# Kernel optimization log

Measured on AMD Instinct MI355X. Metric: run time of the kernel, lower is better.

Reference implementation:

```python
import jax, jax.numpy as jnp
import numpy as np

N, E, G = 100000, 500000, 1000


def _gat(h_in, src, dst, W, a_s, a_d, b, n):
    # PyG GATConv, heads=1, concat=True, negative_slope=0.2, self-loops already in src/dst
    h = h_in @ W.T                                  # [N, out]
    alpha_src = h @ a_s                             # [N]
    alpha_dst = h @ a_d                             # [N]
    e = jax.nn.leaky_relu(alpha_src[src] + alpha_dst[dst], 0.2)  # [E']
    m = jax.ops.segment_max(e, dst, num_segments=n)
    ex = jnp.exp(e - m[dst])
    den = jax.ops.segment_sum(ex, dst, num_segments=n)
    alpha = ex / den[dst]                           # segment softmax over incoming edges
    out = jax.ops.segment_sum(h[src] * alpha[:, None], dst, num_segments=n)
    return out + b


def _forward(x, edge_index, batch, w1, b1, w2, b2, w3, b3,
             g1w, g1as, g1ad, g1b, g2w, g2as, g2ad, g2b,
             g3w, g3as, g3ad, g3b, g4w, g4as, g4ad, g4b,
             g5w, g5as, g5ad, g5b, lw, lb):
    n = x.shape[0]
    h = jax.nn.relu(x @ w1.T + b1)
    h = jax.nn.relu(h @ w2.T + b2)
    h = jax.nn.relu(h @ w3.T + b3)
    loops = jnp.arange(n)
    src = jnp.concatenate([edge_index[0], loops])   # add self-loops
    dst = jnp.concatenate([edge_index[1], loops])
    h = jax.nn.relu(_gat(h, src, dst, g1w, g1as, g1ad, g1b, n))
    h = jax.nn.relu(_gat(h, src, dst, g2w, g2as, g2ad, g2b, n))
    h = jax.nn.relu(_gat(h, src, dst, g3w, g3as, g3ad, g3b, n))
    h = jax.nn.relu(_gat(h, src, dst, g4w, g4as, g4ad, g4b, n))
    h = jax.nn.relu(_gat(h, src, dst, g5w, g5as, g5ad, g5b, n))
    sums = jax.ops.segment_sum(h, batch, num_segments=G)            # [G,32]
    cnt = jax.ops.segment_sum(jnp.ones((n,), h.dtype), batch, num_segments=G)
    mean = sums / jnp.maximum(cnt, 1.0)[:, None]
    return jax.nn.sigmoid(mean @ lw.T + lb)         # [G,1]


def setup_inputs() -> dict:
    key = jax.random.key(0)
    ks = jax.random.split(key, 24)

    def lin(k, o, i):
        k1, k2 = jax.random.split(k)
        s = 1.0 / np.sqrt(i)
        return (jax.random.uniform(k1, (o, i), jnp.float32, -s, s),
                jax.random.uniform(k2, (o,), jnp.float32, -s, s))

    def gat_p(k, i, o):
        k1, k2, k3 = jax.random.split(k, 3)
        s = 1.0 / np.sqrt(i)
        W = jax.random.uniform(k1, (o, i), jnp.float32, -s, s)
        a_s = jax.random.normal(k2, (o,), jnp.float32) / np.sqrt(o)
        a_d = jax.random.normal(k3, (o,), jnp.float32) / np.sqrt(o)
        return W, a_s, a_d, jnp.zeros((o,), jnp.float32)

    inp = {}
    inp['x'] = jax.random.normal(ks[0], (N, 1), jnp.float32)
    inp['edge_index'] = jax.random.randint(ks[1], (2, E), 0, N)
    inp['batch'] = jnp.sort(jax.random.randint(ks[2], (N,), 0, G))
    inp['w1'], inp['b1'] = lin(ks[3], 16, 1)
    inp['w2'], inp['b2'] = lin(ks[4], 32, 16)
    inp['w3'], inp['b3'] = lin(ks[5], 64, 32)
    dims = [(64, 128), (128, 256), (256, 128), (128, 64), (64, 32)]
    for j, (i, o) in enumerate(dims, start=1):
        W, a_s, a_d, b = gat_p(ks[5 + j], i, o)
        inp[f'g{j}w'], inp[f'g{j}as'], inp[f'g{j}ad'], inp[f'g{j}b'] = W, a_s, a_d, b
    inp['lw'], inp['lb'] = lin(ks[12], 1, 32)
    return inp


def reference(x, edge_index, batch, w1, b1, w2, b2, w3, b3,
              g1w, g1as, g1ad, g1b, g2w, g2as, g2ad, g2b,
              g3w, g3as, g3ad, g3b, g4w, g4as, g4ad, g4b,
              g5w, g5as, g5ad, g5b, lw, lb):
    return _forward(x, edge_index, batch, w1, b1, w2, b2, w3, b3,
                    g1w, g1as, g1ad, g1b, g2w, g2as, g2ad, g2b,
                    g3w, g3as, g3ad, g3b, g4w, g4as, g4ad, g4b,
                    g5w, g5as, g5ad, g5b, lw, lb)
```

## Files before the change

kernel.cpp:

```cpp
#include <hip/hip_runtime.h>
#include <math.h>

typedef __attribute__((ext_vector_type(8))) __bf16 bf16x8;
typedef __attribute__((ext_vector_type(4))) float f32x4;

__device__ inline unsigned short f2bf(float f) {
    unsigned int i = __float_as_uint(f);
    unsigned int r = i + 0x7fffu + ((i >> 16) & 1u);
    return (unsigned short)(r >> 16);
}
__device__ inline float bf2f(unsigned short u) {
    return __uint_as_float(((unsigned int)u) << 16);
}

__global__ __launch_bounds__(256) void mlp_kernel(
    const float* __restrict__ x,
    const float* __restrict__ w1, const float* __restrict__ b1,
    const float* __restrict__ w2, const float* __restrict__ b2,
    const float* __restrict__ w3, const float* __restrict__ b3,
    unsigned short* __restrict__ h0, int n,
    const float* __restrict__ g0,
    const float* __restrict__ as1, const float* __restrict__ ad1,
    float* __restrict__ s1out, float* __restrict__ d1out) {
    int tid = threadIdx.x;
    __shared__ float4 sw1q[4], sb1q[4];
    __shared__ float4 sw2q[128];
    __shared__ float4 sw3q[512];
    __shared__ float2 psd1[64];
    __shared__ float sb2l[32], sb3l[64];
    __shared__ float pres[4][64], predu[4][64];
    {
        int ii = tid & 63, ch = tid >> 6;
        const float* gp = g0 + (size_t)(ch * 32) * 64 + ii;
        float s = 0.f, d = 0.f;
#pragma unroll 4
        for (int o = 0; o < 32; o++) {
            float w = gp[o * 64];
            s += as1[ch * 32 + o] * w;
            d += ad1[ch * 32 + o] * w;
        }
        pres[ch][ii] = s;
        predu[ch][ii] = d;
    }
    if (tid < 4) { sw1q[tid] = ((const float4*)w1)[tid]; sb1q[tid] = ((const float4*)b1)[tid]; }
    if (tid >= 32 && tid < 64) sb2l[tid - 32] = b2[tid - 32];
    if (tid >= 64 && tid < 128) sb3l[tid - 64] = b3[tid - 64];
    for (int i = tid; i < 128; i += 256) sw2q[i] = ((const float4*)w2)[i];
    for (int i = tid; i < 512; i += 256) sw3q[i] = ((const float4*)w3)[i];
    __syncthreads();
    if (tid < 64) {
        psd1[tid] = make_float2(pres[0][tid] + pres[1][tid] + pres[2][tid] + pres[3][tid],
                                predu[0][tid] + predu[1][tid] + predu[2][tid] + predu[3][tid]);
    }
    __syncthreads();
    int node = blockIdx.x * 256 + tid;
    if (node >= n) return;
    float xv = x[node];
    float t1[16], t2[32];
#pragma unroll
    for (int q = 0; q < 4; q++) {
        float4 wv = sw1q[q], bv = sb1q[q];
        t1[q * 4 + 0] = fmaxf(wv.x * xv + bv.x, 0.f);
        t1[q * 4 + 1] = fmaxf(wv.y * xv + bv.y, 0.f);
        t1[q * 4 + 2] = fmaxf(wv.z * xv + bv.z, 0.f);
        t1[q * 4 + 3] = fmaxf(wv.w * xv + bv.w, 0.f);
    }
#pragma unroll
    for (int o = 0; o < 32; o++) {
        float a = sb2l[o];
#pragma unroll
        for (int q = 0; q < 4; q++) {
            float4 wv = sw2q[o * 4 + q];
            a += wv.x * t1[q * 4] + wv.y * t1[q * 4 + 1] + wv.z * t1[q * 4 + 2] +
                 wv.w * t1[q * 4 + 3];
        }
        t2[o] = fmaxf(a, 0.f);
    }
    float sdot = 0.f, ddot = 0.f;
    uint4* gp = (uint4*)(h0 + (size_t)node * 64);
#pragma unroll
    for (int c = 0; c < 8; c++) {
        unsigned int wvec[4];
#pragma unroll
        for (int p = 0; p < 4; p++) {
            int o = c * 8 + p * 2;
            float a0 = sb3l[o], a1 = sb3l[o + 1];
#pragma unroll
            for (int q = 0; q < 8; q++) {
                float4 wa = sw3q[o * 8 + q];
                float4 wb = sw3q[(o + 1) * 8 + q];
                a0 += wa.x * t2[q * 4] + wa.y * t2[q * 4 + 1] + wa.z * t2[q * 4 + 2] +
                      wa.w * t2[q * 4 + 3];
                a1 += wb.x * t2[q * 4] + wb.y * t2[q * 4 + 1] + wb.z * t2[q * 4 + 2] +
                      wb.w * t2[q * 4 + 3];
            }
            float r0 = fmaxf(a0, 0.f), r1 = fmaxf(a1, 0.f);
            float2 q0 = psd1[o], q1 = psd1[o + 1];
            sdot += r0 * q0.x + r1 * q1.x;
            ddot += r0 * q0.y + r1 * q1.y;
            wvec[p] = (unsigned)f2bf(r0) | ((unsigned)f2bf(r1) << 16);
        }
        gp[c] = make_uint4(wvec[0], wvec[1], wvec[2], wvec[3]);
    }
    s1out[node] = sdot;
    d1out[node] = ddot;
}

__global__ __launch_bounds__(256) void misc_kernel(
    const float* __restrict__ g0, const float* __restrict__ g1, const float* __restrict__ g2,
    const float* __restrict__ g3, const float* __restrict__ g4,
    unsigned short* __restrict__ wbAll,
    const int* __restrict__ batch, int* __restrict__ gstart, int G, int n,
    const int* __restrict__ dst, int* __restrict__ deg, int E,
    int f2bfB, int gsB, int histB,
    const float* __restrict__ as2, const float* __restrict__ ad2,
    float* __restrict__ pv2) {
    int b = blockIdx.x;
    int tid = threadIdx.x;
    if (b < f2bfB) {
        int i = b * 256 + tid;
        float v;
        if (i < 8192) v = g0[i];
        else if (i < 40960) v = g1[i - 8192];
        else if (i < 73728) v = g2[i - 40960];
        else if (i < 81920) v = g3[i - 73728];
        else if (i < 83968) v = g4[i - 81920];
        else return;
        wbAll[i] = f2bf(v);
    } else if (b < f2bfB + gsB) {
        int g = (b - f2bfB) * 256 + tid;
        if (g > G) return;
        if (g == G) { gstart[G] = n; return; }
        int lo = 0, hi = n;
        while (lo < hi) {
            int mid = (lo + hi) >> 1;
            if (batch[mid] < g) lo = mid + 1;
            else hi = mid;
        }
        gstart[g] = lo;
    } else if (b < f2bfB + gsB + histB) {
        int e = (b - f2bfB - gsB) * 256 + tid;
        if (e >= E) return;
        atomicAdd(&deg[dst[e]], 1);
    } else {
        if (tid < 128) {
            float s = 0.f;
            for (int o = 0; o < 256; o++) s += as2[o] * g1[o * 128 + tid];
            pv2[tid] = s;
        } else {
            int c = tid - 128;
            float s = 0.f;
            for (int o = 0; o < 256; o++) s += ad2[o] * g1[o * 128 + c];
            pv2[128 + c] = s;
        }
    }
}

template <int K, int BN, int EPI>
__global__ __launch_bounds__(256) void gemm_mfma(
    const unsigned short* __restrict__ A, const unsigned short* __restrict__ Wb,
    unsigned short* __restrict__ Cb,
    const float* __restrict__ avs, const float* __restrict__ avd,
    float* __restrict__ as_, float* __restrict__ ad_,
    const float* __restrict__ bias, int n, int O) {
    constexpr int SN = BN / 32;
    constexpr int K8 = K / 8;
    __shared__ unsigned short As[128][K + 8];
    __shared__ unsigned short Ws[BN][72];
    int tid = threadIdx.x;
    int row0 = blockIdx.x * 128;
    int w = tid >> 6, lane = tid & 63;
    int wr = w >> 1, wc = w & 1;
    int quad = lane >> 4, l15 = lane & 15;

    for (int i = tid; i < 128 * K8; i += 256) {
        int r = i / K8, c8 = i % K8;
        int gr = row0 + r;
        uint4 v = make_uint4(0u, 0u, 0u, 0u);
        if (gr < n) v = *(const uint4*)(A + (size_t)gr * K + c8 * 8);
        *(uint4*)&As[r][c8 * 8] = v;
    }

    for (int ot = 0; ot * BN < O; ot++) {
        int col0 = ot * BN;
        f32x4 acc[4][SN];
#pragma unroll
        for (int mi = 0; mi < 4; mi++)
#pragma unroll
            for (int ni = 0; ni < SN; ni++) acc[mi][ni] = (f32x4){0.f, 0.f, 0.f, 0.f};
#pragma unroll 1
        for (int k0 = 0; k0 < K; k0 += 64) {
#pragma unroll
            for (int i = tid; i < BN * 8; i += 256) {
                int r = i >> 3, c8 = i & 7;
                uint4 v = *(const uint4*)(Wb + (size_t)(col0 + r) * K + k0 + c8 * 8);
                *(uint4*)&Ws[r][c8 * 8] = v;
            }
            __syncthreads();
#pragma unroll
            for (int kk = 0; kk < 64; kk += 32) {
                bf16x8 bfr[SN];
#pragma unroll
                for (int ni = 0; ni < SN; ni++)
                    bfr[ni] = *(const bf16x8*)&Ws[wc * (BN / 2) + ni * 16 + l15][kk + quad * 8];
#pragma unroll
                for (int mi = 0; mi < 4; mi++) {
                    bf16x8 afr = *(const bf16x8*)&As[wr * 64 + mi * 16 + l15][k0 + kk + quad * 8];
#pragma unroll
                    for (int ni = 0; ni < SN; ni++)
                        acc[mi][ni] = __builtin_amdgcn_mfma_f32_16x16x32_bf16(
                            afr, bfr[ni], acc[mi][ni], 0, 0, 0);
                }
            }
            __syncthreads();
        }
        float avsv[SN], avdv[SN], bv[SN];
        int gc[SN];
#pragma unroll
        for (int ni = 0; ni < SN; ni++) {
            gc[ni] = col0 + wc * (BN / 2) + ni * 16 + l15;
            if constexpr (EPI != 2) {
                avsv[ni] = avs[gc[ni]];
                avdv[ni] = avd[gc[ni]];
            }
            if constexpr (EPI >= 1) bv[ni] = bias[gc[ni]];
        }
#pragma unroll
        for (int mi = 0; mi < 4; mi++) {
            int gm0 = row0 + wr * 64 + mi * 16 + quad * 4;
            float ps[4] = {0.f, 0.f, 0.f, 0.f}, pd[4] = {0.f, 0.f, 0.f, 0.f};
#pragma unroll
            for (int ni = 0; ni < SN; ni++) {
#pragma unroll
                for (int r = 0; r < 4; r++) {
                    float d = acc[mi][ni][r];
                    if constexpr (EPI >= 1) d = fmaxf(d + bv[ni], 0.f);
                    int gm = gm0 + r;
                    if (gm < n) Cb[(size_t)gm * O + gc[ni]] = f2bf(d);
                    if constexpr (EPI != 2) {
                        ps[r] += d * avsv[ni];
                        pd[r] += d * avdv[ni];
                    }
                }
            }
            if constexpr (EPI != 2) {
#pragma unroll
                for (int r = 0; r < 4; r++) {
#pragma unroll
                    for (int m = 1; m <= 8; m <<= 1) {
                        ps[r] += __shfl_xor(ps[r], m);
                        pd[r] += __shfl_xor(pd[r], m);
                    }
                }
                if (l15 == 0) {
#pragma unroll
                    for (int r = 0; r < 4; r++) {
                        int gm = gm0 + r;
                        if (gm < n) {
                            atomicAdd(&as_[gm], ps[r]);
                            atomicAdd(&ad_[gm], pd[r]);
                        }
                    }
                }
            }
        }
    }
}

__global__ void scan_block_sums(const int* __restrict__ deg, int* __restrict__ bsums, int n) {
    __shared__ int sdata[256];
    int tid = threadIdx.x;
    int base = blockIdx.x * 1024 + tid * 4;
    int s = 0;
    for (int i = 0; i < 4; i++) {
        int g = base + i;
        if (g < n) s += deg[g] + 1;
    }
    sdata[tid] = s;
    __syncthreads();
    for (int off = 128; off > 0; off >>= 1) {
        if (tid < off) sdata[tid] += sdata[tid + off];
        __syncthreads();
    }
    if (tid == 0) bsums[blockIdx.x] = sdata[0];
}

__global__ void scan_write(const int* __restrict__ deg, const int* __restrict__ bsums,
                           int* __restrict__ rowptr, int* __restrict__ cursor,
                           int* __restrict__ esrc, int n, int nb) {
    __shared__ int sdata[256];
    int tid = threadIdx.x;
    sdata[tid] = (tid < blockIdx.x && tid < nb) ? bsums[tid] : 0;
    __syncthreads();
    for (int off = 128; off > 0; off >>= 1) {
        if (tid < off) sdata[tid] += sdata[tid + off];
        __syncthreads();
    }
    int base = sdata[0];
    __syncthreads();
    int gbase = blockIdx.x * 1024 + tid * 4;
    int v[4];
    int s = 0;
    for (int i = 0; i < 4; i++) {
        int g = gbase + i;
        v[i] = (g < n) ? deg[g] + 1 : 0;
        s += v[i];
    }
    sdata[tid] = s;
    __syncthreads();
    for (int off = 1; off < 256; off <<= 1) {
        int t = (tid >= off) ? sdata[tid - off] : 0;
        __syncthreads();
        sdata[tid] += t;
        __syncthreads();
    }
    int excl = sdata[tid] - s + base;
    for (int i = 0; i < 4; i++) {
        int g = gbase + i;
        if (g < n) {
            rowptr[g] = excl;
            esrc[excl] = g;
            cursor[g] = excl + 1;
        }
        excl += v[i];
    }
    if (blockIdx.x == gridDim.x - 1 && tid == 255) rowptr[n] = base + sdata[255];
}

__global__ void scatter_kernel(const int* __restrict__ esrc_in, const int* __restrict__ edst_in,
                               int* __restrict__ cursor, int* __restrict__ esrc, int E) {
    int e = blockIdx.x * 256 + threadIdx.x;
    if (e >= E) return;
    int pos = atomicAdd(&cursor[edst_in[e]], 1);
    esrc[pos] = esrc_in[e];
}

template <int O, bool BIASRELU>
__global__ __launch_bounds__(256) void gat_aggregate(
    const unsigned short* __restrict__ hl, const float* __restrict__ as_,
    const float* __restrict__ ad_, const int* __restrict__ rowptr,
    const int* __restrict__ esrc, const float* __restrict__ bias,
    unsigned short* __restrict__ hout, int n, float* __restrict__ zeroBuf, int zeroCnt) {
    int gtid = blockIdx.x * 256 + threadIdx.x;
    if (gtid < zeroCnt) zeroBuf[gtid] = 0.f;
    constexpr int C8 = O / 8;
    constexpr int EPP = 16 / C8;
    int tid = threadIdx.x;
    int v = blockIdx.x * 16 + (tid >> 4);
    int l = tid & 15;
    int gbase = tid & 48;
    if (v >= n) return;
    int beg = rowptr[v], end = rowptr[v + 1];
    int deg = end - beg;
    float adv = ad_[v];
    int sub = l / C8;
    int c = l % C8;
    float acc[8] = {0.f, 0.f, 0.f, 0.f, 0.f, 0.f, 0.f, 0.f};
    if (deg <= 16) {
        int sreg = v;
        float e = -1e30f;
        if (l < deg) {
            sreg = esrc[beg + l];
            float t = as_[sreg] + adv;
            e = (t > 0.f) ? t : 0.2f * t;
        }
        float m = e;
#pragma unroll
        for (int o = 8; o > 0; o >>= 1) m = fmaxf(m, __shfl_xor(m, o));
        float ex = (l < deg) ? __expf(e - m) : 0.f;
        float sum = ex;
#pragma unroll
        for (int o = 8; o > 0; o >>= 1) sum += __shfl_xor(sum, o);
        float alpha_r = ex / sum;
        for (int j0 = 0; j0 < deg; j0 += EPP) {
            int idx = j0 + sub;
            int cidx = (idx < deg) ? idx : 0;
            float alpha = __shfl(alpha_r, gbase + cidx);
            int s2 = __shfl(sreg, gbase + cidx);
            if (idx >= deg) alpha = 0.f;
            uint4 raw = ((const uint4*)(hl + (size_t)s2 * O))[c];
            acc[0] += alpha * __uint_as_float(raw.x << 16);
            acc[1] += alpha * __uint_as_float(raw.x & 0xffff0000u);
            acc[2] += alpha * __uint_as_float(raw.y << 16);
            acc[3] += alpha * __uint_as_float(raw.y & 0xffff0000u);
            acc[4] += alpha * __uint_as_float(raw.z << 16);
            acc[5] += alpha * __uint_as_float(raw.z & 0xffff0000u);
            acc[6] += alpha * __uint_as_float(raw.w << 16);
            acc[7] += alpha * __uint_as_float(raw.w & 0xffff0000u);
        }
    } else {
        float mymax = -1e30f;
        for (int j = beg + l; j < end; j += 16) {
            float e = as_[esrc[j]] + adv;
            e = (e > 0.f) ? e : 0.2f * e;
            mymax = fmaxf(mymax, e);
        }
#pragma unroll
        for (int o = 8; o > 0; o >>= 1) mymax = fmaxf(mymax, __shfl_xor(mymax, o));
        float mysum = 0.f;
        for (int j = beg + l; j < end; j += 16) {
            float e = as_[esrc[j]] + adv;
            e = (e > 0.f) ? e : 0.2f * e;
            mysum += __expf(e - mymax);
        }
#pragma unroll
        for (int o = 8; o > 0; o >>= 1) mysum += __shfl_xor(mysum, o);
        float invden = 1.f / mysum;
        for (int j0 = beg; j0 < end; j0 += EPP) {
            int j = j0 + sub;
            bool valid = j < end;
            int s = valid ? esrc[j] : v;
            float e = as_[s] + adv;
            e = (e > 0.f) ? e : 0.2f * e;
            float alpha = valid ? __expf(e - mymax) * invden : 0.f;
            uint4 raw = ((const uint4*)(hl + (size_t)s * O))[c];
            acc[0] += alpha * __uint_as_float(raw.x << 16);
            acc[1] += alpha * __uint_as_float(raw.x & 0xffff0000u);
            acc[2] += alpha * __uint_as_float(raw.y << 16);
            acc[3] += alpha * __uint_as_float(raw.y & 0xffff0000u);
            acc[4] += alpha * __uint_as_float(raw.z << 16);
            acc[5] += alpha * __uint_as_float(raw.z & 0xffff0000u);
            acc[6] += alpha * __uint_as_float(raw.w << 16);
            acc[7] += alpha * __uint_as_float(raw.w & 0xffff0000u);
        }
    }
#pragma unroll
    for (int o = C8; o < 16; o <<= 1)
#pragma unroll
        for (int k = 0; k < 8; k++) acc[k] += __shfl_xor(acc[k], o);
    if (l < C8) {
        unsigned short ov[8];
#pragma unroll
        for (int k = 0; k < 8; k++) {
            float val = acc[k];
            if constexpr (BIASRELU) val = fmaxf(val + bias[c * 8 + k], 0.f);
            ov[k] = f2bf(val);
        }
        uint4 packed;
        packed.x = (unsigned)ov[0] | ((unsigned)ov[1] << 16);
        packed.y = (unsigned)ov[2] | ((unsigned)ov[3] << 16);
        packed.z = (unsigned)ov[4] | ((unsigned)ov[5] << 16);
        packed.w = (unsigned)ov[6] | ((unsigned)ov[7] << 16);
        ((uint4*)(hout + (size_t)v * O))[c] = packed;
    }
}

__global__ __launch_bounds__(256) void pool_final_kernel(
    const unsigned short* __restrict__ h, const int* __restrict__ start,
    const float* __restrict__ lw, const float* __restrict__ lb,
    float* __restrict__ out, int G) {
    __shared__ float red[8][33];
    int g = blockIdx.x;
    if (g >= G) return;
    int beg = start[g], end = start[g + 1];
    int tid = threadIdx.x;
    int nodeLane = tid >> 5, f = tid & 31;
    float acc = 0.f;
    for (int v = beg + nodeLane; v < end; v += 8)
        acc += bf2f(h[(size_t)v * 32 + f]);
    red[nodeLane][f] = acc;
    __syncthreads();
    if (tid < 32) {
        float s = 0.f;
#pragma unroll
        for (int i = 0; i < 8; i++) s += red[i][f];
        float inv = 1.f / fmaxf((float)(end - beg), 1.f);
        float val = s * inv * lw[f];
#pragma unroll
        for (int o = 16; o > 0; o >>= 1) val += __shfl_xor(val, o);
        if (f == 0) out[g] = 1.f / (1.f + __expf(-(val + lb[0])));
    }
}

extern "C" void kernel_launch(void* const* d_in, const int* in_sizes, int n_in,
                              void* d_out, int out_size, void* d_ws, size_t ws_size,
                              hipStream_t stream) {
    const float* x = (const float*)d_in[0];
    const int* ei = (const int*)d_in[1];
    const int* batch = (const int*)d_in[2];
    const float* w1 = (const float*)d_in[3];
    const float* b1 = (const float*)d_in[4];
    const float* w2 = (const float*)d_in[5];
    const float* b2 = (const float*)d_in[6];
    const float* w3 = (const float*)d_in[7];
    const float* b3 = (const float*)d_in[8];
    const float* gw[5];
    const float* gas[5];
    const float* gad[5];
    const float* gb[5];
    for (int l = 0; l < 5; l++) {
        gw[l] = (const float*)d_in[9 + l * 4 + 0];
        gas[l] = (const float*)d_in[9 + l * 4 + 1];
        gad[l] = (const float*)d_in[9 + l * 4 + 2];
        gb[l] = (const float*)d_in[9 + l * 4 + 3];
    }
    const float* lw = (const float*)d_in[29];
    const float* lb = (const float*)d_in[30];
    float* out = (float*)d_out;

    int N = in_sizes[0];
    int E = in_sizes[1] / 2;
    int G = out_size;
    int Etot = E + N;

    char* ws = (char*)d_ws;
    size_t off = 0;
    auto alloc = [&](size_t bytes) -> void* {
        void* p = ws + off;
        off = (off + bytes + 255) & ~(size_t)255;
        return p;
    };
    unsigned short* actA = (unsigned short*)alloc((size_t)N * 256 * 2);
    unsigned short* actB = (unsigned short*)alloc((size_t)N * 256 * 2);
    char* zblock = (char*)alloc((size_t)N * 20);
    float* sd2 = (float*)zblock;
    float* sd3 = sd2 + (size_t)N * 2;
    int* deg = (int*)(zblock + (size_t)N * 16);
    float* sd1 = (float*)alloc((size_t)N * 2 * 4);
    float* pv2 = (float*)alloc(256 * 4);
    int* rowptr = (int*)alloc((size_t)(N + 1) * 4);
    int* cursor = (int*)alloc((size_t)(N + 1) * 4);
    int* esrc = (int*)alloc((size_t)Etot * 4);
    int* bsums = (int*)alloc(4096);
    int* gstart = (int*)alloc((size_t)(G + 1) * 4);
    unsigned short* wbAll = (unsigned short*)alloc((size_t)83968 * 2);
    const int woff[5] = {0, 8192, 40960, 73728, 81920};
    unsigned short* wb[5];
    for (int l = 0; l < 5; l++) wb[l] = wbAll + woff[l];
    (void)ws_size;
    (void)n_in;

    hipMemsetAsync(zblock, 0, (size_t)N * 20, stream);

    int f2bfB = (83968 + 255) / 256;
    int gsB = (G + 1 + 255) / 256;
    int histB = (E + 255) / 256;
    misc_kernel<<<f2bfB + gsB + histB + 1, 256, 0, stream>>>(
        gw[0], gw[1], gw[2], gw[3], gw[4], wbAll, batch, gstart, G, N, ei + E, deg, E,
        f2bfB, gsB, histB, gas[1], gad[1], pv2);

    mlp_kernel<<<(N + 255) / 256, 256, 0, stream>>>(x, w1, b1, w2, b2, w3, b3, actA, N,
                                                    gw[0], gas[0], gad[0], sd1, sd1 + N);

    int nb = (N + 1023) / 1024;
    scan_block_sums<<<nb, 256, 0, stream>>>(deg, bsums, N);
    scan_write<<<nb, 256, 0, stream>>>(deg, bsums, rowptr, cursor, esrc, N, nb);
    scatter_kernel<<<(E + 255) / 256, 256, 0, stream>>>(ei, ei + E, cursor, esrc, E);

    int aggBlocks = (N + 15) / 16;
    int gx = (N + 127) / 128;

    gat_aggregate<64, false><<<aggBlocks, 256, 0, stream>>>(
        actA, sd1, sd1 + N, rowptr, esrc, nullptr, actB, N, nullptr, 0);
    gemm_mfma<64, 64, 1><<<gx, 256, 0, stream>>>(actB, wb[0], actA, pv2, pv2 + 128, sd2,
                                                 sd2 + N, gb[0], N, 128);

    gat_aggregate<128, false><<<aggBlocks, 256, 0, stream>>>(
        actA, sd2, sd2 + N, rowptr, esrc, nullptr, actB, N, sd1, 2 * N);
    gemm_mfma<128, 64, 2><<<gx, 256, 0, stream>>>(actB, wb[1], actA, nullptr, nullptr,
                                                  nullptr, nullptr, gb[1], N, 256);

    gemm_mfma<256, 64, 0><<<gx, 256, 0, stream>>>(actA, wb[2], actB, gas[2], gad[2], sd3,
                                                  sd3 + N, nullptr, N, 128);
    gat_aggregate<128, true><<<aggBlocks, 256, 0, stream>>>(
        actB, sd3, sd3 + N, rowptr, esrc, gb[2], actA, N, sd2, 2 * N);

    gemm_mfma<128, 64, 0><<<gx, 256, 0, stream>>>(actA, wb[3], actB, gas[3], gad[3], sd1,
                                                  sd1 + N, nullptr, N, 64);
    gat_aggregate<64, true><<<aggBlocks, 256, 0, stream>>>(
        actB, sd1, sd1 + N, rowptr, esrc, gb[3], actA, N, nullptr, 0);

    gemm_mfma<64, 32, 0><<<gx, 256, 0, stream>>>(actA, wb[4], actB, gas[4], gad[4], sd2,
                                                 sd2 + N, nullptr, N, 32);
    gat_aggregate<32, true><<<aggBlocks, 256, 0, stream>>>(
        actB, sd2, sd2 + N, rowptr, esrc, gb[4], actA, N, nullptr, 0);

    pool_final_kernel<<<G, 256, 0, stream>>>(actA, gstart, lw, lb, out, G);
}
```

Before: 500.9 us.

## Split GEMM output columns across grid.y and stream A tiles per K step

The GEMM kernel used to load a whole 128xK A tile into shared memory once and then loop over all output column tiles inside a single block. It now assigns one column tile per block through a 2D grid and streams 64-wide A chunks per K step. The goal is more blocks in flight and a smaller LDS footprint, which should raise occupancy for the wide layers. In exchange, A is re-read from global memory once per column tile, and K is now a runtime argument rather than a template constant.

```diff
diff --git a/kernel.cpp b/kernel.cpp
--- a/kernel.cpp
+++ b/kernel.cpp
@@ -156,110 +156,105 @@
     }
 }
 
-template <int K, int BN, int EPI>
+template <int BN, int EPI>
 __global__ __launch_bounds__(256) void gemm_mfma(
     const unsigned short* __restrict__ A, const unsigned short* __restrict__ Wb,
     unsigned short* __restrict__ Cb,
     const float* __restrict__ avs, const float* __restrict__ avd,
     float* __restrict__ as_, float* __restrict__ ad_,
-    const float* __restrict__ bias, int n, int O) {
+    const float* __restrict__ bias, int n, int K, int O) {
     constexpr int SN = BN / 32;
-    constexpr int K8 = K / 8;
-    __shared__ unsigned short As[128][K + 8];
+    __shared__ unsigned short As[128][72];
     __shared__ unsigned short Ws[BN][72];
     int tid = threadIdx.x;
-    int row0 = blockIdx.x * 128;
+    int row0 = blockIdx.x * 128, col0 = blockIdx.y * BN;
     int w = tid >> 6, lane = tid & 63;
     int wr = w >> 1, wc = w & 1;
     int quad = lane >> 4, l15 = lane & 15;
-
-    for (int i = tid; i < 128 * K8; i += 256) {
-        int r = i / K8, c8 = i % K8;
-        int gr = row0 + r;
-        uint4 v = make_uint4(0u, 0u, 0u, 0u);
-        if (gr < n) v = *(const uint4*)(A + (size_t)gr * K + c8 * 8);
-        *(uint4*)&As[r][c8 * 8] = v;
-    }
-
-    for (int ot = 0; ot * BN < O; ot++) {
-        int col0 = ot * BN;
-        f32x4 acc[4][SN];
-#pragma unroll
-        for (int mi = 0; mi < 4; mi++)
-#pragma unroll
-            for (int ni = 0; ni < SN; ni++) acc[mi][ni] = (f32x4){0.f, 0.f, 0.f, 0.f};
-#pragma unroll 1
-        for (int k0 = 0; k0 < K; k0 += 64) {
-#pragma unroll
-            for (int i = tid; i < BN * 8; i += 256) {
-                int r = i >> 3, c8 = i & 7;
-                uint4 v = *(const uint4*)(Wb + (size_t)(col0 + r) * K + k0 + c8 * 8);
-                *(uint4*)&Ws[r][c8 * 8] = v;
+    f32x4 acc[4][SN];
+#pragma unroll
+    for (int mi = 0; mi < 4; mi++)
+#pragma unroll
+        for (int ni = 0; ni < SN; ni++) acc[mi][ni] = (f32x4){0.f, 0.f, 0.f, 0.f};
+
+    for (int k0 = 0; k0 < K; k0 += 64) {
+#pragma unroll
+        for (int i = tid; i < 1024; i += 256) {
+            int r = i >> 3, c8 = i & 7;
+            int gr = row0 + r;
+            uint4 v = make_uint4(0u, 0u, 0u, 0u);
+            if (gr < n) v = *(const uint4*)(A + (size_t)gr * K + k0 + c8 * 8);
+            *(uint4*)&As[r][c8 * 8] = v;
+        }
+#pragma unroll
+        for (int i = tid; i < BN * 8; i += 256) {
+            int r = i >> 3, c8 = i & 7;
+            uint4 v = *(const uint4*)(Wb + (size_t)(col0 + r) * K + k0 + c8 * 8);
+            *(uint4*)&Ws[r][c8 * 8] = v;
+        }
+        __syncthreads();
+#pragma unroll
+        for (int kk = 0; kk < 64; kk += 32) {
+            bf16x8 bfr[SN];
+#pragma unroll
+            for (int ni = 0; ni < SN; ni++)
+                bfr[ni] = *(const bf16x8*)&Ws[wc * (BN / 2) + ni * 16 + l15][kk + quad * 8];
+#pragma unroll
+            for (int mi = 0; mi < 4; mi++) {
+                bf16x8 afr = *(const bf16x8*)&As[wr * 64 + mi * 16 + l15][kk + quad * 8];
+#pragma unroll
+                for (int ni = 0; ni < SN; ni++)
+                    acc[mi][ni] = __builtin_amdgcn_mfma_f32_16x16x32_bf16(afr, bfr[ni],
+                                                                          acc[mi][ni], 0, 0, 0);
             }
-            __syncthreads();
-#pragma unroll
-            for (int kk = 0; kk < 64; kk += 32) {
-                bf16x8 bfr[SN];
-#pragma unroll
-                for (int ni = 0; ni < SN; ni++)
-                    bfr[ni] = *(const bf16x8*)&Ws[wc * (BN / 2) + ni * 16 + l15][kk + quad * 8];
-#pragma unroll
-                for (int mi = 0; mi < 4; mi++) {
-                    bf16x8 afr = *(const bf16x8*)&As[wr * 64 + mi * 16 + l15][k0 + kk + quad * 8];
-#pragma unroll
-                    for (int ni = 0; ni < SN; ni++)
-                        acc[mi][ni] = __builtin_amdgcn_mfma_f32_16x16x32_bf16(
-                            afr, bfr[ni], acc[mi][ni], 0, 0, 0);
+        }
+        __syncthreads();
+    }
+    float avsv[SN], avdv[SN], bv[SN];
+    int gc[SN];
+#pragma unroll
+    for (int ni = 0; ni < SN; ni++) {
+        gc[ni] = col0 + wc * (BN / 2) + ni * 16 + l15;
+        if constexpr (EPI != 2) {
+            avsv[ni] = avs[gc[ni]];
+            avdv[ni] = avd[gc[ni]];
+        }
+        if constexpr (EPI >= 1) bv[ni] = bias[gc[ni]];
+    }
+#pragma unroll
+    for (int mi = 0; mi < 4; mi++) {
+        int gm0 = row0 + wr * 64 + mi * 16 + quad * 4;
+        float ps[4] = {0.f, 0.f, 0.f, 0.f}, pd[4] = {0.f, 0.f, 0.f, 0.f};
+#pragma unroll
+        for (int ni = 0; ni < SN; ni++) {
+#pragma unroll
+            for (int r = 0; r < 4; r++) {
+                float d = acc[mi][ni][r];
+                if constexpr (EPI >= 1) d = fmaxf(d + bv[ni], 0.f);
+                int gm = gm0 + r;
+                if (gm < n) Cb[(size_t)gm * O + gc[ni]] = f2bf(d);
+                if constexpr (EPI != 2) {
+                    ps[r] += d * avsv[ni];
+                    pd[r] += d * avdv[ni];
                 }
             }
-            __syncthreads();
-        }
-        float avsv[SN], avdv[SN], bv[SN];
-        int gc[SN];
-#pragma unroll
-        for (int ni = 0; ni < SN; ni++) {
-            gc[ni] = col0 + wc * (BN / 2) + ni * 16 + l15;
-            if constexpr (EPI != 2) {
-                avsv[ni] = avs[gc[ni]];
-                avdv[ni] = avd[gc[ni]];
-            }
-            if constexpr (EPI >= 1) bv[ni] = bias[gc[ni]];
-        }
-#pragma unroll
-        for (int mi = 0; mi < 4; mi++) {
-            int gm0 = row0 + wr * 64 + mi * 16 + quad * 4;
-            float ps[4] = {0.f, 0.f, 0.f, 0.f}, pd[4] = {0.f, 0.f, 0.f, 0.f};
-#pragma unroll
-            for (int ni = 0; ni < SN; ni++) {
-#pragma unroll
-                for (int r = 0; r < 4; r++) {
-                    float d = acc[mi][ni][r];
-                    if constexpr (EPI >= 1) d = fmaxf(d + bv[ni], 0.f);
-                    int gm = gm0 + r;
-                    if (gm < n) Cb[(size_t)gm * O + gc[ni]] = f2bf(d);
-                    if constexpr (EPI != 2) {
-                        ps[r] += d * avsv[ni];
-                        pd[r] += d * avdv[ni];
-                    }
+        }
+        if constexpr (EPI != 2) {
+#pragma unroll
+            for (int r = 0; r < 4; r++) {
+#pragma unroll
+                for (int m = 1; m <= 8; m <<= 1) {
+                    ps[r] += __shfl_xor(ps[r], m);
+                    pd[r] += __shfl_xor(pd[r], m);
                 }
             }
-            if constexpr (EPI != 2) {
+            if (l15 == 0) {
 #pragma unroll
                 for (int r = 0; r < 4; r++) {
-#pragma unroll
-                    for (int m = 1; m <= 8; m <<= 1) {
-                        ps[r] += __shfl_xor(ps[r], m);
-                        pd[r] += __shfl_xor(pd[r], m);
-                    }
-                }
-                if (l15 == 0) {
-#pragma unroll
-                    for (int r = 0; r < 4; r++) {
-                        int gm = gm0 + r;
-                        if (gm < n) {
-                            atomicAdd(&as_[gm], ps[r]);
-                            atomicAdd(&ad_[gm], pd[r]);
-                        }
+                    int gm = gm0 + r;
+                    if (gm < n) {
+                        atomicAdd(&as_[gm], ps[r]);
+                        atomicAdd(&ad_[gm], pd[r]);
                     }
                 }
             }
@@ -552,26 +547,41 @@
 
     gat_aggregate<64, false><<<aggBlocks, 256, 0, stream>>>(
         actA, sd1, sd1 + N, rowptr, esrc, nullptr, actB, N, nullptr, 0);
-    gemm_mfma<64, 64, 1><<<gx, 256, 0, stream>>>(actB, wb[0], actA, pv2, pv2 + 128, sd2,
-                                                 sd2 + N, gb[0], N, 128);
+    {
+        dim3 grid(gx, 2);
+        gemm_mfma<64, 1><<<grid, 256, 0, stream>>>(actB, wb[0], actA, pv2, pv2 + 128, sd2,
+                                                   sd2 + N, gb[0], N, 64, 128);
+    }
 
     gat_aggregate<128, false><<<aggBlocks, 256, 0, stream>>>(
         actA, sd2, sd2 + N, rowptr, esrc, nullptr, actB, N, sd1, 2 * N);
-    gemm_mfma<128, 64, 2><<<gx, 256, 0, stream>>>(actB, wb[1], actA, nullptr, nullptr,
-                                                  nullptr, nullptr, gb[1], N, 256);
-
-    gemm_mfma<256, 64, 0><<<gx, 256, 0, stream>>>(actA, wb[2], actB, gas[2], gad[2], sd3,
-                                                  sd3 + N, nullptr, N, 128);
+    {
+        dim3 grid(gx, 4);
+        gemm_mfma<64, 2><<<grid, 256, 0, stream>>>(actB, wb[1], actA, nullptr, nullptr,
+                                                   nullptr, nullptr, gb[1], N, 128, 256);
+    }
+
+    {
+        dim3 grid(gx, 2);
+        gemm_mfma<64, 0><<<grid, 256, 0, stream>>>(actA, wb[2], actB, gas[2], gad[2], sd3,
+                                                   sd3 + N, nullptr, N, 256, 128);
+    }
     gat_aggregate<128, true><<<aggBlocks, 256, 0, stream>>>(
         actB, sd3, sd3 + N, rowptr, esrc, gb[2], actA, N, sd2, 2 * N);
 
-    gemm_mfma<128, 64, 0><<<gx, 256, 0, stream>>>(actA, wb[3], actB, gas[3], gad[3], sd1,
-                                                  sd1 + N, nullptr, N, 64);
+    {
+        dim3 grid(gx, 1);
+        gemm_mfma<64, 0><<<grid, 256, 0, stream>>>(actA, wb[3], actB, gas[3], gad[3], sd1,
+                                                   sd1 + N, nullptr, N, 128, 64);
+    }
     gat_aggregate<64, true><<<aggBlocks, 256, 0, stream>>>(
         actB, sd1, sd1 + N, rowptr, esrc, gb[3], actA, N, nullptr, 0);
 
-    gemm_mfma<64, 32, 0><<<gx, 256, 0, stream>>>(actA, wb[4], actB, gas[4], gad[4], sd2,
-                                                 sd2 + N, nullptr, N, 32);
+    {
+        dim3 grid(gx, 1);
+        gemm_mfma<32, 0><<<grid, 256, 0, stream>>>(actA, wb[4], actB, gas[4], gad[4], sd2,
+                                                   sd2 + N, nullptr, N, 64, 32);
+    }
     gat_aggregate<32, true><<<aggBlocks, 256, 0, stream>>>(
         actB, sd2, sd2 + N, rowptr, esrc, gb[4], actA, N, nullptr, 0);
 
```

Result: faster. 468.1 us (-6.6%).
